# Kernel tuning notes

Hardware: AMD Instinct MI355X
Metric: run time of the kernel (lower is better)

## Reference

```python
import jax, jax.numpy as jnp
import numpy as np

B, N, D, H = 4, 1024, 1024, 16
DH = D // H  # head dim = 64
SCALE = D ** (-0.5)  # scale_with_head=False -> dim**-0.5


def setup_inputs() -> dict:
    key = jax.random.key(0)
    ks = jax.random.split(key, 6)
    x = jax.random.normal(ks[0], (B, N, D), dtype=jnp.float32)
    mask = jax.random.randint(ks[1], (B, N - 1), 0, 2).astype(bool)
    Wqkv = jax.random.normal(ks[2], (D, 3 * D), dtype=jnp.float32) * (D ** -0.5)
    bqkv = jax.random.normal(ks[3], (3 * D,), dtype=jnp.float32) * 0.02
    Wout = jax.random.normal(ks[4], (D, D), dtype=jnp.float32) * (D ** -0.5)
    bout = jax.random.normal(ks[5], (D,), dtype=jnp.float32) * 0.02
    return {"x": x, "mask": mask, "Wqkv": Wqkv, "bqkv": bqkv, "Wout": Wout, "bout": bout}


def reference(x, mask, Wqkv, bqkv, Wout, bout):
    b, n, _ = x.shape
    qkv = x @ Wqkv + bqkv                      # [b, n, 3D]
    q, k, v = jnp.split(qkv, 3, axis=-1)
    split_heads = lambda t: t.reshape(b, n, H, DH).transpose(0, 2, 1, 3)  # [b,h,n,d]
    q, k, v = split_heads(q), split_heads(k), split_heads(v)
    dots = jnp.einsum('bhid,bhjd->bhij', q, k) * SCALE  # [b,h,n,n]
    mask_value = -jnp.finfo(dots.dtype).max
    # F.pad(mask.flatten(1), (1,0), value=True): prepend one True column
    m = jnp.concatenate([jnp.ones((b, 1), dtype=bool), mask], axis=1)  # [b, n]
    pair = m[:, None, :] & m[:, :, None]       # [b, n, n]
    dots = jnp.where(pair[:, None, :, :], dots, mask_value)
    attn = jax.nn.softmax(dots, axis=-1)
    out = jnp.einsum('bhij,bhjd->bhid', attn, v)
    out = out.transpose(0, 2, 1, 3).reshape(b, n, D)
    out = out @ Wout + bout                    # dropout p=0.0 -> identity
    return (out, attn)
```

## Files before the change

kernel.cpp:

```cpp
#include <hip/hip_runtime.h>
#include <stdint.h>

#define DEV static __device__ __forceinline__

typedef __attribute__((ext_vector_type(8))) __bf16 bfx8;
typedef __attribute__((ext_vector_type(4))) float f32x4;

DEV short f2bfbits(float f) {
  union { float f; unsigned u; } v; v.f = f;
  unsigned r = v.u + 0x7fffu + ((v.u >> 16) & 1u);
  return (short)(r >> 16);
}

DEV void gload_lds16(const void* g, void* lds) {
  __builtin_amdgcn_global_load_lds(
      (const __attribute__((address_space(1))) void*)g,
      (__attribute__((address_space(3))) void*)lds, 16, 0, 0);
}

__global__ void k_prep(const float* __restrict__ src, short* __restrict__ dst,
                       const int* __restrict__ mask, unsigned char* __restrict__ msk) {
  int bx = blockIdx.x;
  if (bx < 4096) {
    int i = bx * 256 + threadIdx.x;
    float4 v = ((const float4*)src)[i];
    union { short s[4]; uint64_t u; } o;
    o.s[0] = f2bfbits(v.x); o.s[1] = f2bfbits(v.y);
    o.s[2] = f2bfbits(v.z); o.s[3] = f2bfbits(v.w);
    ((uint64_t*)dst)[i] = o.u;
  } else {
    int i = (bx - 4096) * 256 + threadIdx.x;
    int b = i >> 10, n = i & 1023;
    msk[i] = (n == 0) ? (unsigned char)1 : (unsigned char)(mask[b * 1023 + n - 1] != 0);
  }
}

__global__ void k_transpose2(const float* __restrict__ Wqkv, short* __restrict__ wqkvT,
                             const float* __restrict__ Wout, short* __restrict__ woutT) {
  __shared__ float tile[32][33];
  int bx = blockIdx.x;
  const float* src; short* dst; int C;
  if (bx < 96) { src = Wqkv; dst = wqkvT; C = 3072; }
  else         { src = Wout; dst = woutT; C = 1024; bx -= 96; }
  const int R = 1024;
  int c0 = bx * 32, r0 = blockIdx.y * 32;
  int tx = threadIdx.x, ty = threadIdx.y;
  #pragma unroll
  for (int j = 0; j < 32; j += 8)
    tile[ty + j][tx] = src[(size_t)(r0 + ty + j) * C + c0 + tx];
  __syncthreads();
  #pragma unroll
  for (int j = 0; j < 32; j += 8)
    dst[(size_t)(c0 + ty + j) * R + r0 + tx] = f2bfbits(tile[tx][ty + j]);
}

__global__ __launch_bounds__(256)
void k_gemm(const short* __restrict__ A, const short* __restrict__ Bt,
            const float* __restrict__ bias, int K,
            short* __restrict__ qf, short* __restrict__ kf,
            short* __restrict__ vf) {
  __shared__ short As[128 * 32];
  __shared__ short Bs[128 * 32];
  const int t = threadIdx.x;
  const int l = t & 63, w = t >> 6;
  const int lr = l & 15, lk = l >> 4;
  const int m0 = blockIdx.y * 128, n0 = blockIdx.x * 128;
  const int wr = (w >> 1) * 64, wc = (w & 1) * 64;
  f32x4 acc[4][4] = {};

  const int srow = t >> 2;
  const int sc8 = (t & 3) * 8;
  const size_t aoff1 = (size_t)(m0 + srow) * K + sc8;
  const size_t aoff2 = (size_t)(m0 + srow + 64) * K + sc8;
  const size_t boff1 = (size_t)(n0 + srow) * K + sc8;
  const size_t boff2 = (size_t)(n0 + srow + 64) * K + sc8;
  short* asd1 = As + (t & ~63) * 8;
  short* asd2 = As + (t & ~63) * 8 + 2048;
  short* bsd1 = Bs + (t & ~63) * 8;
  short* bsd2 = Bs + (t & ~63) * 8 + 2048;

  for (int k0 = 0; k0 < K; k0 += 32) {
    gload_lds16(A + aoff1 + k0, asd1);
    gload_lds16(A + aoff2 + k0, asd2);
    gload_lds16(Bt + boff1 + k0, bsd1);
    gload_lds16(Bt + boff2 + k0, bsd2);
    __syncthreads();
    bfx8 af[4], bf[4];
    #pragma unroll
    for (int m = 0; m < 4; m++)
      af[m] = *(const bfx8*)&As[(wr + m * 16 + lr) * 32 + lk * 8];
    #pragma unroll
    for (int n = 0; n < 4; n++)
      bf[n] = *(const bfx8*)&Bs[(wc + n * 16 + lr) * 32 + lk * 8];
    #pragma unroll
    for (int m = 0; m < 4; m++)
      #pragma unroll
      for (int n = 0; n < 4; n++)
        acc[m][n] = __builtin_amdgcn_mfma_f32_16x16x32_bf16(af[m], bf[n], acc[m][n], 0, 0, 0);
    __syncthreads();
  }

  #pragma unroll
  for (int m = 0; m < 4; m++) {
    int grb = m0 + wr + m * 16 + 4 * lk;
    #pragma unroll
    for (int n = 0; n < 4; n++) {
      int gc = n0 + wc + n * 16 + lr;
      float bv = bias[gc];
      int which = gc >> 10, rem = gc & 1023;
      int hh = rem >> 6, dd = rem & 63;
      #pragma unroll
      for (int i = 0; i < 4; i++) {
        int gr = grb + i;
        int bb = gr >> 10, nn = gr & 1023;
        size_t bh = (size_t)(bb * 16 + hh);
        short val = f2bfbits(acc[m][n][i] + bv);
        if (which < 2) {
          size_t idx = ((bh * 64 + (nn >> 4)) << 10) + ((size_t)(dd >> 5) << 9) +
                       ((((dd >> 3) & 3) * 16 + (nn & 15)) << 3) + (dd & 7);
          if (which == 0) qf[idx] = val; else kf[idx] = val;
        } else {
          size_t idx = (((bh * 4 + (dd >> 4)) * 32 + (nn >> 5)) << 9) +
                       ((((nn >> 3) & 3) * 16 + (dd & 15)) << 3) + (nn & 7);
          vf[idx] = val;
        }
      }
    }
  }
}

__global__ __launch_bounds__(256)
void k_gemm_out(const short* __restrict__ A, const short* __restrict__ Bt,
                const float* __restrict__ bias, float* __restrict__ outF) {
  __shared__ short As[128 * 32];
  __shared__ short Bs[64 * 32];
  const int K = 1024;
  const int t = threadIdx.x;
  const int l = t & 63, w = t >> 6;
  const int lr = l & 15, lk = l >> 4;
  const int m0 = blockIdx.y * 128, n0 = blockIdx.x * 64;
  const int wr = (w >> 1) * 64, wc = (w & 1) * 32;
  f32x4 acc[4][2] = {};

  const int srow = t >> 2;
  const int sc8 = (t & 3) * 8;
  const size_t aoff1 = (size_t)(m0 + srow) * K + sc8;
  const size_t aoff2 = (size_t)(m0 + srow + 64) * K + sc8;
  const size_t boff1 = (size_t)(n0 + srow) * K + sc8;
  short* asd1 = As + (t & ~63) * 8;
  short* asd2 = As + (t & ~63) * 8 + 2048;
  short* bsd1 = Bs + (t & ~63) * 8;

  for (int k0 = 0; k0 < K; k0 += 32) {
    gload_lds16(A + aoff1 + k0, asd1);
    gload_lds16(A + aoff2 + k0, asd2);
    gload_lds16(Bt + boff1 + k0, bsd1);
    __syncthreads();
    bfx8 af[4], bf[2];
    #pragma unroll
    for (int m = 0; m < 4; m++)
      af[m] = *(const bfx8*)&As[(wr + m * 16 + lr) * 32 + lk * 8];
    #pragma unroll
    for (int n = 0; n < 2; n++)
      bf[n] = *(const bfx8*)&Bs[(wc + n * 16 + lr) * 32 + lk * 8];
    #pragma unroll
    for (int m = 0; m < 4; m++)
      #pragma unroll
      for (int n = 0; n < 2; n++)
        acc[m][n] = __builtin_amdgcn_mfma_f32_16x16x32_bf16(af[m], bf[n], acc[m][n], 0, 0, 0);
    __syncthreads();
  }

  #pragma unroll
  for (int m = 0; m < 4; m++) {
    #pragma unroll
    for (int n = 0; n < 2; n++) {
      int gc = n0 + wc + n * 16 + lr;
      float bv = bias[gc];
      #pragma unroll
      for (int i = 0; i < 4; i++) {
        int gr = m0 + wr + m * 16 + 4 * lk + i;
        outF[(size_t)gr * 1024 + gc] = acc[m][n][i] + bv;
      }
    }
  }
}

__global__ __launch_bounds__(512, 4)
void k_attn(const short* __restrict__ qf_, const short* __restrict__ kf_,
            const short* __restrict__ vf_, const unsigned char* __restrict__ msk,
            float* __restrict__ attn, short* __restrict__ ctx) {
  __shared__ short P[16 * 1024];
  __shared__ float redM[16][8];
  __shared__ float redS[16][8];
  __shared__ f32x4 redC[256];
  const int t = threadIdx.x, l = t & 63, w = t >> 6;
  const int lr = l & 15, lk = l >> 4;
  const int wg = ((blockIdx.x & 7) << 9) | (blockIdx.x >> 3);
  const int rt = wg & 63, h = (wg >> 6) & 15, b = wg >> 10;
  const int bh = b * 16 + h;
  const int r0 = rt * 16;
  const float NEG = -3.402823466e38f;

  const short* qf = qf_ + ((size_t)(bh * 64 + rt) << 10);
  bfx8 aq0 = *(const bfx8*)&qf[l * 8];
  bfx8 aq1 = *(const bfx8*)&qf[512 + l * 8];

  const unsigned char* mb = msk + b * 1024;
  const bool rowok = mb[r0 + lr] != 0;

  f32x4 sc[8];
  #pragma unroll
  for (int cc = 0; cc < 8; cc++) {
    const short* kfp = kf_ + ((size_t)(bh * 64 + w * 8 + cc) << 10);
    bfx8 bk0 = *(const bfx8*)&kfp[l * 8];
    bfx8 bk1 = *(const bfx8*)&kfp[512 + l * 8];
    f32x4 a = {};
    a = __builtin_amdgcn_mfma_f32_16x16x32_bf16(bk0, aq0, a, 0, 0, 0);
    a = __builtin_amdgcn_mfma_f32_16x16x32_bf16(bk1, aq1, a, 0, 0, 0);
    unsigned cm = *(const unsigned*)&mb[w * 128 + cc * 16 + 4 * lk];
    #pragma unroll
    for (int i = 0; i < 4; i++) {
      bool ok = rowok && (((cm >> (8 * i)) & 0xffu) != 0u);
      sc[cc][i] = ok ? a[i] * 0.03125f : NEG;
    }
  }

  float m = NEG;
  #pragma unroll
  for (int f = 0; f < 8; f++)
    #pragma unroll
    for (int i = 0; i < 4; i++) m = fmaxf(m, sc[f][i]);
  m = fmaxf(m, __shfl_xor(m, 16));
  m = fmaxf(m, __shfl_xor(m, 32));
  if (lk == 0) redM[lr][w] = m;
  __syncthreads();
  {
    float4 m0 = *(const float4*)&redM[lr][0];
    float4 m1 = *(const float4*)&redM[lr][4];
    m = fmaxf(fmaxf(fmaxf(m0.x, m0.y), fmaxf(m0.z, m0.w)),
              fmaxf(fmaxf(m1.x, m1.y), fmaxf(m1.z, m1.w)));
  }
  float s = 0.f;
  #pragma unroll
  for (int f = 0; f < 8; f++)
    #pragma unroll
    for (int i = 0; i < 4; i++) { sc[f][i] = __expf(sc[f][i] - m); s += sc[f][i]; }
  s += __shfl_xor(s, 16);
  s += __shfl_xor(s, 32);
  if (lk == 0) redS[lr][w] = s;
  __syncthreads();
  float inv;
  {
    float4 s0 = *(const float4*)&redS[lr][0];
    float4 s1 = *(const float4*)&redS[lr][4];
    inv = 1.0f / (s0.x + s0.y + s0.z + s0.w + s1.x + s1.y + s1.z + s1.w);
  }

  #pragma unroll
  for (int cc = 0; cc < 8; cc++) {
    union { ushort u[4]; uint2 d; } pk;
    pk.u[0] = (ushort)f2bfbits(sc[cc][0] * inv);
    pk.u[1] = (ushort)f2bfbits(sc[cc][1] * inv);
    pk.u[2] = (ushort)f2bfbits(sc[cc][2] * inv);
    pk.u[3] = (ushort)f2bfbits(sc[cc][3] * inv);
    int slot_lin = w * 16 + cc * 2 + (lk >> 1);
    int addr = lr * 2048 + ((slot_lin ^ (lr & 7)) << 4) + ((lk & 1) << 3);
    *(uint2*)((char*)P + addr) = pk.d;
  }
  __syncthreads();

  #pragma unroll
  for (int rg = 0; rg < 2; rg++) {
    int row = w * 2 + rg;
    float* arow = attn + ((size_t)bh * 1024 + r0 + row) * 1024;
    int swr = row & 7;
    #pragma unroll
    for (int it = 0; it < 4; it++) {
      int ci = it * 64 + l;
      uint2 d = *(const uint2*)((const char*)P + row * 2048 +
                                (((ci >> 1) ^ swr) << 4) + ((ci & 1) << 3));
      float4 o;
      o.x = __uint_as_float(d.x << 16);
      o.y = __uint_as_float(d.x & 0xffff0000u);
      o.z = __uint_as_float(d.y << 16);
      o.w = __uint_as_float(d.y & 0xffff0000u);
      *(float4*)&arow[ci * 4] = o;
    }
  }

  const int dg = w & 3, ch = w >> 2;
  f32x4 o0 = {}, o1 = {};
  #pragma unroll
  for (int j = 0; j < 16; j++) {
    int jj = ch * 16 + j;
    const short* vfp = vf_ + (((size_t)(bh * 4 + dg) * 32 + jj) << 9);
    bfx8 bv = *(const bfx8*)&vfp[l * 8];
    int slot_lin = jj * 4 + lk;
    bfx8 pa = *(const bfx8*)((const char*)P + lr * 2048 +
                             ((slot_lin ^ (lr & 7)) << 4));
    if (j & 1) o1 = __builtin_amdgcn_mfma_f32_16x16x32_bf16(pa, bv, o1, 0, 0, 0);
    else       o0 = __builtin_amdgcn_mfma_f32_16x16x32_bf16(pa, bv, o0, 0, 0, 0);
  }

  f32x4 oo;
  #pragma unroll
  for (int i = 0; i < 4; i++) oo[i] = o0[i] + o1[i];
  if (w >= 4) redC[(w - 4) * 64 + l] = oo;
  __syncthreads();
  if (w < 4) {
    f32x4 op = redC[w * 64 + l];
    #pragma unroll
    for (int i = 0; i < 4; i++) {
      float v = oo[i] + op[i];
      ctx[(((size_t)b << 10) + r0 + 4 * lk + i) * 1024 + (h << 6) + (w << 4) + lr] =
          f2bfbits(v);
    }
  }
}


extern "C" void kernel_launch(void* const* d_in, const int* in_sizes, int n_in,
                              void* d_out, int out_size, void* d_ws, size_t ws_size,
                              hipStream_t stream) {
  const float* x    = (const float*)d_in[0];
  const int*   mask = (const int*)d_in[1];
  const float* Wqkv = (const float*)d_in[2];
  const float* bqkv = (const float*)d_in[3];
  const float* Wout = (const float*)d_in[4];
  const float* bout = (const float*)d_in[5];
  float* out  = (float*)d_out;
  float* attn = out + (size_t)4 * 1024 * 1024;

  char* ws = (char*)d_ws;
  short* xb    = (short*)(ws);
  short* wqkvT = (short*)(ws + 8388608);
  short* woutT = (short*)(ws + 14680064);
  short* qfr   = (short*)(ws + 16777216);
  short* kfr   = (short*)(ws + 25165824);
  short* vfr   = (short*)(ws + 33554432);
  short* ctx   = (short*)(ws + 41943040);
  unsigned char* msk = (unsigned char*)(ws + 50331648);

  k_prep<<<4112, 256, 0, stream>>>(x, xb, mask, msk);
  k_transpose2<<<dim3(128, 32), dim3(32, 8), 0, stream>>>(Wqkv, wqkvT, Wout, woutT);
  k_gemm<<<dim3(24, 32), 256, 0, stream>>>(xb, wqkvT, bqkv, 1024, qfr, kfr, vfr);
  k_attn<<<4096, 512, 0, stream>>>(qfr, kfr, vfr, msk, attn, ctx);
  k_gemm_out<<<dim3(16, 32), 256, 0, stream>>>(ctx, woutT, bout, out);
}
```

Measured before the change: 149.1 us.

## Stage QKV epilogue through LDS for coalesced stores and merge prep kernels

The QKV GEMM epilogue used to write each bf16 element to global memory with scattered 2-byte stores into the fragment layouts. It now stages the tile into shared memory in the target layout and writes out contiguous 16-byte vectors, in two passes with barriers between them. The weight transpose kernel is also folded into the prep kernel, saving one launch. The staged epilogue adds barriers and extra LDS traffic, and it relies on each tile mapping exactly onto whole heads.

```diff
diff --git a/kernel.cpp b/kernel.cpp
--- a/kernel.cpp
+++ b/kernel.cpp
@@ -18,40 +18,41 @@
       (__attribute__((address_space(3))) void*)lds, 16, 0, 0);
 }
 
-__global__ void k_prep(const float* __restrict__ src, short* __restrict__ dst,
-                       const int* __restrict__ mask, unsigned char* __restrict__ msk) {
+__global__ void k_prep(const float* __restrict__ x, short* __restrict__ xb,
+                       const int* __restrict__ mask, unsigned char* __restrict__ msk,
+                       const float* __restrict__ Wqkv, short* __restrict__ wqkvT,
+                       const float* __restrict__ Wout, short* __restrict__ woutT) {
+  __shared__ float tile[32][33];
   int bx = blockIdx.x;
+  int t = threadIdx.x;
   if (bx < 4096) {
-    int i = bx * 256 + threadIdx.x;
-    float4 v = ((const float4*)src)[i];
+    int i = bx * 256 + t;
+    float4 v = ((const float4*)x)[i];
     union { short s[4]; uint64_t u; } o;
     o.s[0] = f2bfbits(v.x); o.s[1] = f2bfbits(v.y);
     o.s[2] = f2bfbits(v.z); o.s[3] = f2bfbits(v.w);
-    ((uint64_t*)dst)[i] = o.u;
-  } else {
-    int i = (bx - 4096) * 256 + threadIdx.x;
+    ((uint64_t*)xb)[i] = o.u;
+  } else if (bx < 4112) {
+    int i = (bx - 4096) * 256 + t;
     int b = i >> 10, n = i & 1023;
     msk[i] = (n == 0) ? (unsigned char)1 : (unsigned char)(mask[b * 1023 + n - 1] != 0);
-  }
-}
-
-__global__ void k_transpose2(const float* __restrict__ Wqkv, short* __restrict__ wqkvT,
-                             const float* __restrict__ Wout, short* __restrict__ woutT) {
-  __shared__ float tile[32][33];
-  int bx = blockIdx.x;
-  const float* src; short* dst; int C;
-  if (bx < 96) { src = Wqkv; dst = wqkvT; C = 3072; }
-  else         { src = Wout; dst = woutT; C = 1024; bx -= 96; }
-  const int R = 1024;
-  int c0 = bx * 32, r0 = blockIdx.y * 32;
-  int tx = threadIdx.x, ty = threadIdx.y;
-  #pragma unroll
-  for (int j = 0; j < 32; j += 8)
-    tile[ty + j][tx] = src[(size_t)(r0 + ty + j) * C + c0 + tx];
-  __syncthreads();
-  #pragma unroll
-  for (int j = 0; j < 32; j += 8)
-    dst[(size_t)(c0 + ty + j) * R + r0 + tx] = f2bfbits(tile[tx][ty + j]);
+  } else {
+    int tb = bx - 4112;
+    int bxx = tb & 127, byy = tb >> 7;
+    const float* src; short* dst; int C;
+    if (bxx < 96) { src = Wqkv; dst = wqkvT; C = 3072; }
+    else          { src = Wout; dst = woutT; C = 1024; bxx -= 96; }
+    const int R = 1024;
+    int c0 = bxx * 32, r0 = byy * 32;
+    int tx = t & 31, ty = t >> 5;
+    #pragma unroll
+    for (int j = 0; j < 32; j += 8)
+      tile[ty + j][tx] = src[(size_t)(r0 + ty + j) * C + c0 + tx];
+    __syncthreads();
+    #pragma unroll
+    for (int j = 0; j < 32; j += 8)
+      dst[(size_t)(c0 + ty + j) * R + r0 + tx] = f2bfbits(tile[tx][ty + j]);
+  }
 }
 
 __global__ __launch_bounds__(256)
@@ -59,8 +60,9 @@
             const float* __restrict__ bias, int K,
             short* __restrict__ qf, short* __restrict__ kf,
             short* __restrict__ vf) {
-  __shared__ short As[128 * 32];
-  __shared__ short Bs[128 * 32];
+  __shared__ short smem[8192];
+  short* As = smem;
+  short* Bs = smem + 4096;
   const int t = threadIdx.x;
   const int l = t & 63, w = t >> 6;
   const int lr = l & 15, lk = l >> 4;
@@ -100,32 +102,59 @@
     __syncthreads();
   }
 
-  #pragma unroll
-  for (int m = 0; m < 4; m++) {
-    int grb = m0 + wr + m * 16 + 4 * lk;
-    #pragma unroll
-    for (int n = 0; n < 4; n++) {
-      int gc = n0 + wc + n * 16 + lr;
-      float bv = bias[gc];
-      int which = gc >> 10, rem = gc & 1023;
-      int hh = rem >> 6, dd = rem & 63;
-      #pragma unroll
-      for (int i = 0; i < 4; i++) {
-        int gr = grb + i;
-        int bb = gr >> 10, nn = gr & 1023;
-        size_t bh = (size_t)(bb * 16 + hh);
-        short val = f2bfbits(acc[m][n][i] + bv);
-        if (which < 2) {
-          size_t idx = ((bh * 64 + (nn >> 4)) << 10) + ((size_t)(dd >> 5) << 9) +
-                       ((((dd >> 3) & 3) * 16 + (nn & 15)) << 3) + (dd & 7);
-          if (which == 0) qf[idx] = val; else kf[idx] = val;
-        } else {
-          size_t idx = (((bh * 4 + (dd >> 4)) * 32 + (nn >> 5)) << 9) +
-                       ((((nn >> 3) & 3) * 16 + (dd & 15)) << 3) + (nn & 7);
-          vf[idx] = val;
+  const int which = n0 >> 10;
+  const int head = w & 1;
+  const int band = w >> 1;
+  const int bb = m0 >> 10;
+  const int bh = bb * 16 + ((n0 & 1023) >> 6) + head;
+  short* dstp = (which == 0) ? qf : (which == 1) ? kf : vf;
+
+  #pragma unroll
+  for (int p = 0; p < 2; p++) {
+    #pragma unroll
+    for (int mm = 0; mm < 2; mm++) {
+      int m = 2 * p + mm;
+      #pragma unroll
+      for (int n = 0; n < 4; n++) {
+        int gc = n0 + wc + n * 16 + lr;
+        float bv = bias[gc];
+        #pragma unroll
+        for (int i = 0; i < 4; i++) {
+          short val = f2bfbits(acc[m][n][i] + bv);
+          int off;
+          if (which < 2) {
+            off = ((((band * 2 + head) * 2 + mm) * 2 + (n >> 1)) * 64 +
+                   ((2 * n + (lr >> 3)) & 3) * 16 + 4 * lk + i) * 8 + (lr & 7);
+          } else {
+            off = (((band * 2 + head) * 4 + n) * 64 +
+                   (2 * mm + ((4 * lk + i) >> 3)) * 16 + lr) * 8 + ((4 * lk + i) & 7);
+          }
+          smem[off] = val;
         }
       }
     }
+    __syncthreads();
+    if (which < 2) {
+      #pragma unroll
+      for (int r = 0; r < 4; r++) {
+        int rb = r >> 1, rh = r & 1;
+        int bh_r = bb * 16 + ((n0 & 1023) >> 6) + rh;
+        int blk0 = ((m0 & 1023) >> 4) + 4 * rb + 2 * p;
+        size_t g = ((size_t)(bh_r * 64 + blk0) << 10) + t * 8;
+        *(int4*)&dstp[g] = *(const int4*)&smem[r * 2048 + t * 8];
+      }
+    } else {
+      #pragma unroll
+      for (int r = 0; r < 4; r++) {
+        int rb = r >> 1, rh = r & 1;
+        int bh_r = bb * 16 + ((n0 & 1023) >> 6) + rh;
+        int jj = ((m0 & 1023) >> 5) + 2 * rb + p;
+        int db = t >> 6;
+        size_t g = (((size_t)(bh_r * 4 + db) * 32 + jj) << 9) + (t & 63) * 8;
+        *(int4*)&dstp[g] = *(const int4*)&smem[r * 2048 + t * 8];
+      }
+    }
+    if (p == 0) __syncthreads();
   }
 }
 
@@ -342,8 +371,7 @@
   short* ctx   = (short*)(ws + 41943040);
   unsigned char* msk = (unsigned char*)(ws + 50331648);
 
-  k_prep<<<4112, 256, 0, stream>>>(x, xb, mask, msk);
-  k_transpose2<<<dim3(128, 32), dim3(32, 8), 0, stream>>>(Wqkv, wqkvT, Wout, woutT);
+  k_prep<<<8208, 256, 0, stream>>>(x, xb, mask, msk, Wqkv, wqkvT, Wout, woutT);
   k_gemm<<<dim3(24, 32), 256, 0, stream>>>(xb, wqkvT, bqkv, 1024, qfr, kfr, vfr);
   k_attn<<<4096, 512, 0, stream>>>(qfr, kfr, vfr, msk, attn, ctx);
   k_gemm_out<<<dim3(16, 32), 256, 0, stream>>>(ctx, woutT, bout, out);
```

New measurement: 144.5 us. 1.03x faster.
